# Optimization experiments

Measured on AMD Instinct MI355X. Metric: run time of the kernel, lower is better.

The kernel has to match this reference:

```python
import jax, jax.numpy as jnp
import numpy as np

B, C, S = 256, 1024, 14   # batch, channels, spatial (frozen by y.view(b,c,14,14))
C2 = 15                   # channels2 in the module
CAT = C // 2 * 3 + C2     # 1551 = 15 + 512 + 1024
EPS = 1e-5


def _conv(x, w, b, groups, pad):
    out = jax.lax.conv_general_dilated(
        x, w, window_strides=(1, 1), padding=((pad, pad), (pad, pad)),
        dimension_numbers=('NCHW', 'OIHW', 'NCHW'), feature_group_count=groups)
    return out + b[None, :, None, None]


def _bn(x, gamma, beta):
    # training-mode BatchNorm2d: biased batch stats over (N,H,W)
    m = x.mean((0, 2, 3), keepdims=True)
    v = x.var((0, 2, 3), keepdims=True)
    return (x - m) * jax.lax.rsqrt(v + EPS) * gamma[None, :, None, None] + beta[None, :, None, None]


def setup_inputs() -> dict:
    key = jax.random.key(0)
    ks = jax.random.split(key, 16)
    r = C2 // 7  # = 2
    inp = {
        'y': jax.random.normal(ks[0], (B, C2, S * S), jnp.float32),
        'x': jax.random.normal(ks[1], (B, C, S, S), jnp.float32),
        'fc1_w': jax.random.normal(ks[2], (r, C2), jnp.float32) * 0.2,
        'fc2_w': jax.random.normal(ks[3], (C2, r), jnp.float32) * 0.2,
        'conv_w': jax.random.normal(ks[4], (C // 2, C, 1, 1), jnp.float32) * 0.03,
        'conv_b': jnp.zeros((C // 2,), jnp.float32),
        'dconv_w': jax.random.normal(ks[5], (C, 1, 3, 3), jnp.float32) * 0.2,
        'dconv_b': jnp.zeros((C,), jnp.float32),
        'dw1_w': jax.random.normal(ks[6], (CAT, 1, 3, 3), jnp.float32) * 0.2,
        'dw1_b': jnp.zeros((CAT,), jnp.float32),
        'pw1_w': jax.random.normal(ks[7], (C // 2, CAT, 1, 1), jnp.float32) * 0.03,
        'pw1_b': jnp.zeros((C // 2,), jnp.float32),
        'gamma': jnp.ones((C // 2,), jnp.float32),
        'beta': jnp.zeros((C // 2,), jnp.float32),
        'n': 0,
    }
    return inp


def reference(y, x, fc1_w, fc2_w, conv_w, conv_b, dconv_w, dconv_b,
              dw1_w, dw1_b, pw1_w, pw1_b, gamma, beta, n):
    b = y.shape[0]
    y4 = y.reshape(b, C2, S, S)
    # SE block on the 15 sub-channels
    g = y4.mean((2, 3))                              # (b, 15) global avg pool
    h = jax.nn.relu(g @ fc1_w.T) @ fc2_w.T           # (b, 15)
    y1 = y4 * jax.nn.sigmoid(h)[:, :, None, None]
    # depthwise conv on x, then per-(b,c) row covariance of the 14x14 map
    x1 = _conv(x, dconv_w, dconv_b, C, 1)            # (b, C, 14, 14)
    x2 = jax.lax.stop_gradient(x1)                   # .detach() in the original
    xc = x2 - x2.mean(-1, keepdims=True)             # np.cov: rows=vars, cols=obs
    cov = jnp.einsum('bcik,bcjk->bcij', xc, xc) / (S - 1)
    z = _conv(cov, conv_w, conv_b, 1, 0)             # 1x1 conv C -> C//2
    z = jax.nn.sigmoid(_bn(z, gamma, beta))
    for _ in range(n):                               # n=0 at these shapes
        y1 = jax.image.resize(y1, (y1.shape[0], y1.shape[1], y1.shape[2] * 2, y1.shape[3] * 2), 'bilinear')
    cat = jnp.concatenate([y1, z, x], axis=1)        # (b, 1551, 14, 14)
    o = _conv(cat, dw1_w, dw1_b, CAT, 1)             # depthwise 3x3
    o = _conv(o, pw1_w, pw1_b, 1, 0)                 # pointwise 1x1 -> C//2
    return jax.nn.relu(_bn(o, gamma, beta))
```

## Files before the change

kernel.cpp:

```cpp
#include <hip/hip_runtime.h>

typedef unsigned int u32;
typedef unsigned short u16;
typedef __attribute__((ext_vector_type(8))) short bf16x8;
typedef __attribute__((ext_vector_type(4))) float f32x4;
typedef __attribute__((ext_vector_type(4))) u32 u32x4;

#define EPSBN 1e-5f

#define GLDS16(gp, lp) __builtin_amdgcn_global_load_lds( \
    (const __attribute__((address_space(1))) u32*)(gp), \
    (__attribute__((address_space(3))) u32*)(lp), 16, 0, 0)

#define OFF_ADW    0ull
#define OFF_COVT   0ull
#define OFF_S      160563200ull
#define OFF_WBZ    160578560ull
#define OFF_WBP    161627136ull
#define OFF_STATSZ 163265536ull
#define OFF_STATSO 163269632ull
#define OFF_SCZ    163273728ull
#define OFF_SHZ    163275776ull
#define OFF_SCO    163277824ull
#define OFF_SHO    163279872ull

static __device__ __forceinline__ float bf2f(u16 h){
  u32 u = ((u32)h) << 16; float f; __builtin_memcpy(&f, &u, 4); return f;
}
static __device__ __forceinline__ u16 f2bf(float f){
  u32 u; __builtin_memcpy(&u, &f, 4);
  u = (u + 0x7fffu + ((u >> 16) & 1u)) >> 16;
  return (u16)u;
}

__global__ __launch_bounds__(64) void se_kernel(const float* __restrict__ y,
    const float* __restrict__ fc1, const float* __restrict__ fc2, float* __restrict__ sse){
  __shared__ float g[15];
  __shared__ float t[2];
  int b = blockIdx.x, l = threadIdx.x;
  for (int c = 0; c < 15; ++c){
    float p = 0.f;
    for (int k = l; k < 196; k += 64) p += y[((size_t)b*15 + c)*196 + k];
    p += __shfl_xor(p, 32); p += __shfl_xor(p, 16); p += __shfl_xor(p, 8);
    p += __shfl_xor(p, 4);  p += __shfl_xor(p, 2);  p += __shfl_xor(p, 1);
    if (l == 0) g[c] = p * (1.f/196.f);
  }
  __syncthreads();
  if (l < 2){
    float a = 0.f;
    for (int c = 0; c < 15; ++c) a += g[c] * fc1[l*15 + c];
    t[l] = fmaxf(a, 0.f);
  }
  __syncthreads();
  if (l < 15){
    float h = t[0]*fc2[l*2] + t[1]*fc2[l*2+1];
    sse[b*15 + l] = 1.f / (1.f + __expf(-h));
  }
}

__global__ void wconv_kernel(const float* __restrict__ cw, const float* __restrict__ pw,
                             u16* __restrict__ wbz, u16* __restrict__ wbp){
  u32 stride = gridDim.x * blockDim.x;
  for (u32 i = blockIdx.x*blockDim.x + threadIdx.x; i < 524288u; i += stride)
    wbz[i] = f2bf(cw[i]);
  for (u32 i = blockIdx.x*blockDim.x + threadIdx.x; i < 819200u; i += stride){
    u32 n = i / 1600u, k = i - n*1600u;
    wbp[i] = f2bf(k < 1551u ? pw[(size_t)n*1551 + k] : 0.f);
  }
}

static __device__ __forceinline__ void dw3x3_row(const float* __restrict__ m,
    int i, const float* __restrict__ w, float bias, float* __restrict__ ov){
  float r[3][14];
  #pragma unroll
  for (int d = 0; d < 3; ++d){
    int rr = i + d - 1;
    if (rr >= 0 && rr < 14){
      #pragma unroll
      for (int k = 0; k < 14; ++k) r[d][k] = m[rr*14 + k];
    } else {
      #pragma unroll
      for (int k = 0; k < 14; ++k) r[d][k] = 0.f;
    }
  }
  #pragma unroll
  for (int k = 0; k < 14; ++k){
    float a = bias;
    #pragma unroll
    for (int dy = 0; dy < 3; ++dy){
      #pragma unroll
      for (int dx = 0; dx < 3; ++dx){
        int kk = k + dx - 1;
        if (kk >= 0 && kk < 14) a += w[dy*3+dx] * r[dy][kk];
      }
    }
    ov[k] = a;
  }
}

__global__ __launch_bounds__(256,5) void cov_kernel(const float* __restrict__ x,
    const float* __restrict__ dcw, const float* __restrict__ dcb, u16* __restrict__ covT){
  __shared__ __align__(16) float xs[16*200];
  __shared__ __align__(16) u32 xcb[16*132];
  __shared__ float wls[16][9];
  __shared__ float wlb[16];
  u32* covL32 = (u32*)xs;

  int tid = threadIdx.x;
  int c0 = blockIdx.x * 16, b = blockIdx.y;

  {
    const float4* xg = (const float4*)(x + ((size_t)b*1024 + c0)*196);
    for (int i = tid; i < 784; i += 256){
      float4 v = xg[i];
      u32 c = (u32)i / 49u, p4 = (u32)i - c*49u;
      *(float4*)&xs[c*200u + p4*4u] = v;
    }
  }
  if (tid < 144) wls[tid/9][tid%9] = dcw[(size_t)(c0 + tid/9)*9 + (tid%9)];
  if (tid < 16) wlb[tid] = dcb[c0 + tid];
  __syncthreads();

  {
    int c = tid >> 4, i = tid & 15;
    u32 q[8];
    #pragma unroll
    for (int j = 0; j < 8; ++j) q[j] = 0u;
    if (i < 14){
      float wr[9];
      #pragma unroll
      for (int qq = 0; qq < 9; ++qq) wr[qq] = wls[c][qq];
      float topm = (i > 0) ? 1.f : 0.f, botm = (i < 13) ? 1.f : 0.f;
      wr[0] *= topm; wr[1] *= topm; wr[2] *= topm;
      wr[6] *= botm; wr[7] *= botm; wr[8] *= botm;
      float bb = wlb[c];
      float rr[3][16];
      #pragma unroll
      for (int d = 0; d < 3; ++d){
        rr[d][0] = 0.f; rr[d][15] = 0.f;
        int rowr = i + d - 1;
        rowr = rowr < 0 ? 0 : (rowr > 13 ? 13 : rowr);
        const float* src = &xs[c*200 + rowr*14];
        #pragma unroll
        for (int j = 0; j < 7; ++j)
          *(float2*)&rr[d][1 + 2*j] = *(const float2*)&src[2*j];
      }
      float ov[14];
      #pragma unroll
      for (int k = 0; k < 14; ++k){
        float a = bb;
        #pragma unroll
        for (int dy = 0; dy < 3; ++dy)
          #pragma unroll
          for (int dx = 0; dx < 3; ++dx)
            a += wr[dy*3+dx] * rr[dy][k + dx];
        ov[k] = a;
      }
      float mean = 0.f;
      #pragma unroll
      for (int k = 0; k < 14; ++k) mean += ov[k];
      mean *= (1.f/14.f);
      #pragma unroll
      for (int j = 0; j < 7; ++j){
        u32 lo = f2bf(ov[2*j]   - mean);
        u32 hi = f2bf(ov[2*j+1] - mean);
        q[j] = lo | (hi << 16);
      }
    }
    u32x4 q0 = {q[0], q[1], q[2], q[3]};
    u32x4 q1 = {q[4], q[5], q[6], q[7]};
    *(u32x4*)&xcb[c*132 + i*8]     = q0;
    *(u32x4*)&xcb[c*132 + i*8 + 4] = q1;
  }
  __syncthreads();

  {
    int w = tid >> 6, l = tid & 63, lr = l & 15, lq = l >> 4;
    #pragma unroll
    for (int pp = 0; pp < 2; ++pp){
      int clo = w*4 + 2*pp;
      bf16x8 alo = {0,0,0,0,0,0,0,0}, ahi = {0,0,0,0,0,0,0,0};
      if (lq < 2){
        alo = *(const bf16x8*)&xcb[clo*132 + lr*8 + lq*4];
        ahi = *(const bf16x8*)&xcb[(clo+1)*132 + lr*8 + lq*4];
      }
      f32x4 dlo = {0.f,0.f,0.f,0.f}, dhi = {0.f,0.f,0.f,0.f};
      dlo = __builtin_amdgcn_mfma_f32_16x16x32_bf16(alo, alo, dlo, 0, 0, 0);
      dhi = __builtin_amdgcn_mfma_f32_16x16x32_bf16(ahi, ahi, dhi, 0, 0, 0);
      if (lr < 14){
        int cp = w*2 + pp;
        #pragma unroll
        for (int r = 0; r < 4; ++r){
          int rowi = lq*4 + r;
          if (rowi < 14){
            u32 vv = (u32)f2bf(dlo[r] * (1.f/13.f)) | ((u32)f2bf(dhi[r] * (1.f/13.f)) << 16);
            covL32[cp*210 + rowi*14 + lr] = vv;
          }
        }
      }
    }
  }
  __syncthreads();

  for (int i = tid; i < 1568; i += 256){
    int cp = i & 7, ij = i >> 3;
    u32 v = covL32[cp*210 + ij];
    *(u32*)(covT + ((size_t)(b*196 + ij)*1024 + c0 + 2*cp)) = v;
  }
}

__global__ __launch_bounds__(256,5) void adw_kernel(
    const float* __restrict__ y, const float* __restrict__ sse,
    const u16* __restrict__ zraw, const float* __restrict__ scz, const float* __restrict__ shz,
    const float* __restrict__ x, const float* __restrict__ dw1w, const float* __restrict__ dw1b,
    u16* __restrict__ Adw){
  __shared__ __align__(16) float ms[32*201 + 4];
  __shared__ float wd[32][9];
  __shared__ float bd[32];
  int tid = threadIdx.x;
  int cc0 = blockIdx.x * 32, b = blockIdx.y;

  for (int i = tid; i < 288; i += 256){
    int c = i / 9, q = i - c*9;
    int cc = cc0 + c;
    wd[c][q] = (cc < 1551) ? dw1w[(size_t)cc*9 + q] : 0.f;
  }
  if (tid < 32) bd[tid] = (cc0 + tid < 1551) ? dw1b[cc0 + tid] : 0.f;

  if (cc0 < 15){
    int ny = 15 - cc0; if (ny > 32) ny = 32;
    for (int i = tid; i < ny*196; i += 256){
      u32 c = (u32)i / 196u, p = (u32)i - c*196u;
      int cc = cc0 + (int)c;
      ms[c*201u + p] = y[((size_t)b*15 + cc)*196 + p] * sse[b*15 + cc];
    }
  }
  {
    int zs = cc0 > 15 ? cc0 : 15;
    int ze = cc0 + 32 < 527 ? cc0 + 32 : 527;
    if (zs < ze){
      int nz = ze - zs, lbase = zs - cc0, obase = zs - 15;
      for (int i = tid; i < nz*196; i += 256){
        int oo = i % nz, p = i / nz;
        int o = obase + oo;
        float v = bf2f(zraw[((size_t)b*196 + p)*512 + o]);
        v = v * scz[o] + shz[o];
        v = 1.f / (1.f + __expf(-v));
        ms[(u32)(lbase + oo)*201u + p] = v;
      }
    }
  }
  {
    int xs_ = cc0 > 527 ? cc0 : 527;
    int xe = cc0 + 32 < 1551 ? cc0 + 32 : 1551;
    if (xs_ < xe){
      int nx = xe - xs_, lbase = xs_ - cc0, cxs = xs_ - 527;
      for (int i = tid; i < nx*196; i += 256){
        u32 c = (u32)i / 196u, p = (u32)i - c*196u;
        ms[(u32)(lbase + (int)c)*201u + p] = x[((size_t)b*1024 + cxs + c)*196 + p];
      }
    }
  }
  {
    int ps = cc0 > 1551 ? cc0 : 1551;
    int pe = cc0 + 32;
    if (ps < pe){
      int np = pe - ps, lbase = ps - cc0;
      for (int i = tid; i < np*196; i += 256){
        u32 c = (u32)i / 196u, p = (u32)i - c*196u;
        ms[(u32)(lbase + (int)c)*201u + p] = 0.f;
      }
    }
  }
  __syncthreads();

  for (int t = tid; t < 448; t += 256){
    int cc = t & 31, i = t >> 5;
    float ov[14];
    dw3x3_row(&ms[cc*201], i, &wd[cc][0], bd[cc], ov);
    size_t obase = ((size_t)b*196 + i*14) * 1600 + cc0 + cc;
    #pragma unroll
    for (int k = 0; k < 14; ++k) Adw[obase + (size_t)k*1600] = f2bf(ov[k]);
  }
}

template<int MODE>
__global__ __launch_bounds__(256,3) void gemm_kernel(
    const u16* __restrict__ A, const u16* __restrict__ Bw,
    const float* __restrict__ bias, void* __restrict__ outp,
    float* __restrict__ stats, int K){
  __shared__ __align__(16) char smem[33280];
  u16* As = (u16*)smem;
  u16* Bs = (u16*)(smem + 16384);

  int tid = threadIdx.x;
  int w = tid >> 6, l = tid & 63;
  int wm = w >> 1, wn = w & 1;
  int lr = l & 15, lq = l >> 4;
  int m0 = blockIdx.y * 128;
  int n0 = blockIdx.x * 128;

  f32x4 acc[4][4] = {};
  int kTiles = K >> 6;

  for (int kt = 0; kt < kTiles; ++kt){
    if (kt) __syncthreads();
    #pragma unroll
    for (int i = 0; i < 4; ++i){
      int s = tid + i*256;
      int row = s >> 3, c8 = s & 7, sc = c8 ^ (row & 7);
      GLDS16(A  + (size_t)(m0 + row)*K + kt*64 + sc*8, As + s*8);
      GLDS16(Bw + (size_t)(n0 + row)*K + kt*64 + sc*8, Bs + s*8);
    }
    __syncthreads();
    #pragma unroll
    for (int ks = 0; ks < 2; ++ks){
      bf16x8 af[4], bfv[4];
      #pragma unroll
      for (int mi = 0; mi < 4; ++mi){
        int row = wm*64 + mi*16 + lr;
        int q = (ks*4 + lq) ^ (row & 7);
        af[mi] = *(const bf16x8*)(As + row*64 + q*8);
      }
      #pragma unroll
      for (int ni = 0; ni < 4; ++ni){
        int row = wn*64 + ni*16 + lr;
        int q = (ks*4 + lq) ^ (row & 7);
        bfv[ni] = *(const bf16x8*)(Bs + row*64 + q*8);
      }
      #pragma unroll
      for (int mi = 0; mi < 4; ++mi)
        #pragma unroll
        for (int ni = 0; ni < 4; ++ni)
          acc[mi][ni] = __builtin_amdgcn_mfma_f32_16x16x32_bf16(af[mi], bfv[ni], acc[mi][ni], 0, 0, 0);
    }
  }

  #pragma unroll
  for (int ni = 0; ni < 4; ++ni){
    int col = n0 + wn*64 + ni*16 + lr;
    float bb = bias[col];
    float s1 = 0.f, s2 = 0.f;
    #pragma unroll
    for (int mi = 0; mi < 4; ++mi)
      #pragma unroll
      for (int r = 0; r < 4; ++r){
        float v = acc[mi][ni][r] + bb;
        acc[mi][ni][r] = v;
        s1 += v; s2 += v*v;
      }
    s1 += __shfl_xor(s1, 16); s1 += __shfl_xor(s1, 32);
    s2 += __shfl_xor(s2, 16); s2 += __shfl_xor(s2, 32);
    if (lq == 0){
      atomicAdd(&stats[col], s1);
      atomicAdd(&stats[512 + col], s2);
    }
  }

  if (MODE == 0){
    u16* zo = (u16*)outp;
    #pragma unroll
    for (int mi = 0; mi < 4; ++mi)
      #pragma unroll
      for (int r = 0; r < 4; ++r){
        int m = m0 + wm*64 + mi*16 + lq*4 + r;
        size_t base = (size_t)m*512 + n0 + wn*64 + lr;
        #pragma unroll
        for (int ni = 0; ni < 4; ++ni)
          zo[base + ni*16] = f2bf(acc[mi][ni][r]);
      }
  } else {
    __syncthreads();
    float* eb = (float*)smem;
    #pragma unroll
    for (int rnd = 0; rnd < 2; ++rnd){
      if (wm == rnd){
        float* e = eb + wn * (64*65);
        #pragma unroll
        for (int mi = 0; mi < 4; ++mi)
          #pragma unroll
          for (int ni = 0; ni < 4; ++ni)
            #pragma unroll
            for (int r = 0; r < 4; ++r)
              e[(mi*16 + lq*4 + r)*65 + ni*16 + lr] = acc[mi][ni][r];
        int m = m0 + wm*64 + l;
        u32 bq = (u32)m / 196u;
        u32 ij = (u32)m - bq*196u;
        float* ob = (float*)outp + ((size_t)bq*512 + n0 + wn*64)*196 + ij;
        #pragma unroll 8
        for (int no = 0; no < 64; ++no)
          ob[(size_t)no*196] = e[l*65 + no];
      }
      __syncthreads();
    }
  }
}

__global__ void bnprep_kernel(const float* __restrict__ stats, const float* __restrict__ gamma,
    const float* __restrict__ beta, float* __restrict__ sc, float* __restrict__ sh){
  int o = threadIdx.x;
  float m = stats[o] * (1.f/50176.f);
  float v = stats[512+o] * (1.f/50176.f) - m*m;
  float inv = rsqrtf(v + EPSBN);
  float g = gamma[o] * inv;
  sc[o] = g;
  sh[o] = beta[o] - m*g;
}

__global__ void final_kernel(float4* __restrict__ o4, const float* __restrict__ sc,
                             const float* __restrict__ sh){
  u32 stride = gridDim.x * blockDim.x;
  for (u32 i = blockIdx.x*blockDim.x + threadIdx.x; i < 6422528u; i += stride){
    u32 oc = (i / 49u) & 511u;
    float s = sc[oc], t = sh[oc];
    float4 v = o4[i];
    v.x = fmaxf(fmaf(v.x, s, t), 0.f);
    v.y = fmaxf(fmaf(v.y, s, t), 0.f);
    v.z = fmaxf(fmaf(v.z, s, t), 0.f);
    v.w = fmaxf(fmaf(v.w, s, t), 0.f);
    o4[i] = v;
  }
}

extern "C" void kernel_launch(void* const* d_in, const int* in_sizes, int n_in,
                              void* d_out, int out_size, void* d_ws, size_t ws_size,
                              hipStream_t stream){
  (void)in_sizes; (void)n_in; (void)out_size; (void)ws_size;
  const float* y      = (const float*)d_in[0];
  const float* x      = (const float*)d_in[1];
  const float* fc1    = (const float*)d_in[2];
  const float* fc2    = (const float*)d_in[3];
  const float* convw  = (const float*)d_in[4];
  const float* convb  = (const float*)d_in[5];
  const float* dconvw = (const float*)d_in[6];
  const float* dconvb = (const float*)d_in[7];
  const float* dw1w   = (const float*)d_in[8];
  const float* dw1b   = (const float*)d_in[9];
  const float* pw1w   = (const float*)d_in[10];
  const float* pw1b   = (const float*)d_in[11];
  const float* gamma  = (const float*)d_in[12];
  const float* beta   = (const float*)d_in[13];

  char* ws = (char*)d_ws;
  u16* covT   = (u16*)(ws + OFF_COVT);
  u16* Adw    = (u16*)(ws + OFF_ADW);
  float* sse  = (float*)(ws + OFF_S);
  u16* wbz    = (u16*)(ws + OFF_WBZ);
  u16* wbp    = (u16*)(ws + OFF_WBP);
  float* statsZ = (float*)(ws + OFF_STATSZ);
  float* statsO = (float*)(ws + OFF_STATSO);
  float* scz  = (float*)(ws + OFF_SCZ);
  float* shz  = (float*)(ws + OFF_SHZ);
  float* sco  = (float*)(ws + OFF_SCO);
  float* sho  = (float*)(ws + OFF_SHO);
  u16* zraw   = (u16*)d_out;
  float* outf = (float*)d_out;

  hipMemsetAsync(statsZ, 0, 8192, stream);
  se_kernel<<<256, 64, 0, stream>>>(y, fc1, fc2, sse);
  wconv_kernel<<<2048, 256, 0, stream>>>(convw, pw1w, wbz, wbp);
  cov_kernel<<<dim3(64, 256), 256, 0, stream>>>(x, dconvw, dconvb, covT);
  gemm_kernel<0><<<dim3(4, 392), 256, 0, stream>>>(covT, wbz, convb, (void*)zraw, statsZ, 1024);
  bnprep_kernel<<<1, 512, 0, stream>>>(statsZ, gamma, beta, scz, shz);
  adw_kernel<<<dim3(50, 256), 256, 0, stream>>>(y, sse, zraw, scz, shz, x, dw1w, dw1b, Adw);
  gemm_kernel<1><<<dim3(4, 392), 256, 0, stream>>>(Adw, wbp, pw1b, (void*)outf, statsO, 1600);
  bnprep_kernel<<<1, 512, 0, stream>>>(statsO, gamma, beta, sco, sho);
  final_kernel<<<8192, 256, 0, stream>>>((float4*)outf, sco, sho);
}
```

Before: 542.1 us.

## Store z channel-major and vectorize adw staging and depthwise stencil

The first GEMM now writes its bf16 z output transposed (channel-major, stride 50176) through the LDS epilogue, the same path the second GEMM already uses. This lets adw_kernel read z as contiguous pixel pairs per channel instead of strided gathers across 512-wide rows. adw also loads x with float4 and pads the LDS row stride to 202 so float2 accesses stay aligned. The 3x3 depthwise stencil uses zero-padded register rows with masked weights instead of per-element branches. The cost is that the z GEMM epilogue now goes through LDS, and its global stores are strided per lane (coalesced across lanes only along m).

```diff
diff --git a/kernel.cpp b/kernel.cpp
--- a/kernel.cpp
+++ b/kernel.cpp
@@ -69,35 +69,6 @@
   }
 }
 
-static __device__ __forceinline__ void dw3x3_row(const float* __restrict__ m,
-    int i, const float* __restrict__ w, float bias, float* __restrict__ ov){
-  float r[3][14];
-  #pragma unroll
-  for (int d = 0; d < 3; ++d){
-    int rr = i + d - 1;
-    if (rr >= 0 && rr < 14){
-      #pragma unroll
-      for (int k = 0; k < 14; ++k) r[d][k] = m[rr*14 + k];
-    } else {
-      #pragma unroll
-      for (int k = 0; k < 14; ++k) r[d][k] = 0.f;
-    }
-  }
-  #pragma unroll
-  for (int k = 0; k < 14; ++k){
-    float a = bias;
-    #pragma unroll
-    for (int dy = 0; dy < 3; ++dy){
-      #pragma unroll
-      for (int dx = 0; dx < 3; ++dx){
-        int kk = k + dx - 1;
-        if (kk >= 0 && kk < 14) a += w[dy*3+dx] * r[dy][kk];
-      }
-    }
-    ov[k] = a;
-  }
-}
-
 __global__ __launch_bounds__(256,5) void cov_kernel(const float* __restrict__ x,
     const float* __restrict__ dcw, const float* __restrict__ dcb, u16* __restrict__ covT){
   __shared__ __align__(16) float xs[16*200];
@@ -211,10 +182,10 @@
 
 __global__ __launch_bounds__(256,5) void adw_kernel(
     const float* __restrict__ y, const float* __restrict__ sse,
-    const u16* __restrict__ zraw, const float* __restrict__ scz, const float* __restrict__ shz,
+    const u16* __restrict__ zT, const float* __restrict__ scz, const float* __restrict__ shz,
     const float* __restrict__ x, const float* __restrict__ dw1w, const float* __restrict__ dw1b,
     u16* __restrict__ Adw){
-  __shared__ __align__(16) float ms[32*201 + 4];
+  __shared__ __align__(16) float ms[32*202];
   __shared__ float wd[32][9];
   __shared__ float bd[32];
   int tid = threadIdx.x;
@@ -228,11 +199,10 @@
   if (tid < 32) bd[tid] = (cc0 + tid < 1551) ? dw1b[cc0 + tid] : 0.f;
 
   if (cc0 < 15){
-    int ny = 15 - cc0; if (ny > 32) ny = 32;
+    int ny = 15;
     for (int i = tid; i < ny*196; i += 256){
       u32 c = (u32)i / 196u, p = (u32)i - c*196u;
-      int cc = cc0 + (int)c;
-      ms[c*201u + p] = y[((size_t)b*15 + cc)*196 + p] * sse[b*15 + cc];
+      ms[c*202u + p] = y[((size_t)b*15 + c)*196 + p] * sse[b*15 + c];
     }
   }
   {
@@ -240,13 +210,18 @@
     int ze = cc0 + 32 < 527 ? cc0 + 32 : 527;
     if (zs < ze){
       int nz = ze - zs, lbase = zs - cc0, obase = zs - 15;
-      for (int i = tid; i < nz*196; i += 256){
-        int oo = i % nz, p = i / nz;
-        int o = obase + oo;
-        float v = bf2f(zraw[((size_t)b*196 + p)*512 + o]);
-        v = v * scz[o] + shz[o];
-        v = 1.f / (1.f + __expf(-v));
-        ms[(u32)(lbase + oo)*201u + p] = v;
+      const u16* zrow = zT + (size_t)obase*50176 + (size_t)b*196;
+      for (int i = tid; i < nz*98; i += 256){
+        u32 oo = (u32)i / 98u, pp = (u32)i - oo*98u;
+        u32 v = *(const u32*)(zrow + (size_t)oo*50176 + pp*2u);
+        int o = obase + (int)oo;
+        float s = scz[o], h = shz[o];
+        float v0 = bf2f((u16)(v & 0xffffu)) * s + h;
+        float v1 = bf2f((u16)(v >> 16))     * s + h;
+        v0 = 1.f / (1.f + __expf(-v0));
+        v1 = 1.f / (1.f + __expf(-v1));
+        float2 fv = {v0, v1};
+        *(float2*)&ms[(u32)(lbase + (int)oo)*202u + pp*2u] = fv;
       }
     }
   }
@@ -255,9 +230,14 @@
     int xe = cc0 + 32 < 1551 ? cc0 + 32 : 1551;
     if (xs_ < xe){
       int nx = xe - xs_, lbase = xs_ - cc0, cxs = xs_ - 527;
-      for (int i = tid; i < nx*196; i += 256){
-        u32 c = (u32)i / 196u, p = (u32)i - c*196u;
-        ms[(u32)(lbase + (int)c)*201u + p] = x[((size_t)b*1024 + cxs + c)*196 + p];
+      const float4* xg = (const float4*)(x + ((size_t)b*1024 + cxs)*196);
+      for (int i = tid; i < nx*49; i += 256){
+        float4 v = xg[i];
+        u32 c = (u32)i / 49u, p4 = (u32)i - c*49u;
+        float* dst = &ms[(u32)(lbase + (int)c)*202u + p4*4u];
+        float2 lo = {v.x, v.y}, hi = {v.z, v.w};
+        *(float2*)dst = lo;
+        *(float2*)(dst + 2) = hi;
       }
     }
   }
@@ -268,7 +248,7 @@
       int np = pe - ps, lbase = ps - cc0;
       for (int i = tid; i < np*196; i += 256){
         u32 c = (u32)i / 196u, p = (u32)i - c*196u;
-        ms[(u32)(lbase + (int)c)*201u + p] = 0.f;
+        ms[(u32)(lbase + (int)c)*202u + p] = 0.f;
       }
     }
   }
@@ -276,11 +256,35 @@
 
   for (int t = tid; t < 448; t += 256){
     int cc = t & 31, i = t >> 5;
-    float ov[14];
-    dw3x3_row(&ms[cc*201], i, &wd[cc][0], bd[cc], ov);
+    float wr[9];
+    #pragma unroll
+    for (int qq = 0; qq < 9; ++qq) wr[qq] = wd[cc][qq];
+    float topm = (i > 0) ? 1.f : 0.f, botm = (i < 13) ? 1.f : 0.f;
+    wr[0] *= topm; wr[1] *= topm; wr[2] *= topm;
+    wr[6] *= botm; wr[7] *= botm; wr[8] *= botm;
+    float bb = bd[cc];
+    float rr[3][16];
+    #pragma unroll
+    for (int d = 0; d < 3; ++d){
+      rr[d][0] = 0.f; rr[d][15] = 0.f;
+      int rowr = i + d - 1;
+      rowr = rowr < 0 ? 0 : (rowr > 13 ? 13 : rowr);
+      const float* src = &ms[cc*202 + rowr*14];
+      #pragma unroll
+      for (int j = 0; j < 7; ++j)
+        *(float2*)&rr[d][1 + 2*j] = *(const float2*)&src[2*j];
+    }
     size_t obase = ((size_t)b*196 + i*14) * 1600 + cc0 + cc;
     #pragma unroll
-    for (int k = 0; k < 14; ++k) Adw[obase + (size_t)k*1600] = f2bf(ov[k]);
+    for (int k = 0; k < 14; ++k){
+      float a = bb;
+      #pragma unroll
+      for (int dy = 0; dy < 3; ++dy)
+        #pragma unroll
+        for (int dx = 0; dx < 3; ++dx)
+          a += wr[dy*3+dx] * rr[dy][k + dx];
+      Adw[obase + (size_t)k*1600] = f2bf(a);
+    }
   }
 }
 
@@ -357,33 +361,26 @@
     }
   }
 
-  if (MODE == 0){
-    u16* zo = (u16*)outp;
-    #pragma unroll
-    for (int mi = 0; mi < 4; ++mi)
-      #pragma unroll
-      for (int r = 0; r < 4; ++r){
-        int m = m0 + wm*64 + mi*16 + lq*4 + r;
-        size_t base = (size_t)m*512 + n0 + wn*64 + lr;
+  __syncthreads();
+  float* eb = (float*)smem;
+  #pragma unroll
+  for (int rnd = 0; rnd < 2; ++rnd){
+    if (wm == rnd){
+      float* e = eb + wn * (64*65);
+      #pragma unroll
+      for (int mi = 0; mi < 4; ++mi)
         #pragma unroll
         for (int ni = 0; ni < 4; ++ni)
-          zo[base + ni*16] = f2bf(acc[mi][ni][r]);
-      }
-  } else {
-    __syncthreads();
-    float* eb = (float*)smem;
-    #pragma unroll
-    for (int rnd = 0; rnd < 2; ++rnd){
-      if (wm == rnd){
-        float* e = eb + wn * (64*65);
-        #pragma unroll
-        for (int mi = 0; mi < 4; ++mi)
           #pragma unroll
-          for (int ni = 0; ni < 4; ++ni)
-            #pragma unroll
-            for (int r = 0; r < 4; ++r)
-              e[(mi*16 + lq*4 + r)*65 + ni*16 + lr] = acc[mi][ni][r];
-        int m = m0 + wm*64 + l;
+          for (int r = 0; r < 4; ++r)
+            e[(mi*16 + lq*4 + r)*65 + ni*16 + lr] = acc[mi][ni][r];
+      int m = m0 + wm*64 + l;
+      if (MODE == 0){
+        u16* ob = (u16*)outp + (size_t)(n0 + wn*64)*50176 + m;
+        #pragma unroll 8
+        for (int no = 0; no < 64; ++no)
+          ob[(size_t)no*50176] = f2bf(e[l*65 + no]);
+      } else {
         u32 bq = (u32)m / 196u;
         u32 ij = (u32)m - bq*196u;
         float* ob = (float*)outp + ((size_t)bq*512 + n0 + wn*64)*196 + ij;
@@ -391,8 +388,8 @@
         for (int no = 0; no < 64; ++no)
           ob[(size_t)no*196] = e[l*65 + no];
       }
-      __syncthreads();
-    }
+    }
+    __syncthreads();
   }
 }
 
@@ -453,16 +450,16 @@
   float* shz  = (float*)(ws + OFF_SHZ);
   float* sco  = (float*)(ws + OFF_SCO);
   float* sho  = (float*)(ws + OFF_SHO);
-  u16* zraw   = (u16*)d_out;
+  u16* zT     = (u16*)d_out;
   float* outf = (float*)d_out;
 
   hipMemsetAsync(statsZ, 0, 8192, stream);
   se_kernel<<<256, 64, 0, stream>>>(y, fc1, fc2, sse);
   wconv_kernel<<<2048, 256, 0, stream>>>(convw, pw1w, wbz, wbp);
   cov_kernel<<<dim3(64, 256), 256, 0, stream>>>(x, dconvw, dconvb, covT);
-  gemm_kernel<0><<<dim3(4, 392), 256, 0, stream>>>(covT, wbz, convb, (void*)zraw, statsZ, 1024);
+  gemm_kernel<0><<<dim3(4, 392), 256, 0, stream>>>(covT, wbz, convb, (void*)zT, statsZ, 1024);
   bnprep_kernel<<<1, 512, 0, stream>>>(statsZ, gamma, beta, scz, shz);
-  adw_kernel<<<dim3(50, 256), 256, 0, stream>>>(y, sse, zraw, scz, shz, x, dw1w, dw1b, Adw);
+  adw_kernel<<<dim3(50, 256), 256, 0, stream>>>(y, sse, zT, scz, shz, x, dw1w, dw1b, Adw);
   gemm_kernel<1><<<dim3(4, 392), 256, 0, stream>>>(Adw, wbp, pw1b, (void*)outf, statsO, 1600);
   bnprep_kernel<<<1, 512, 0, stream>>>(statsO, gamma, beta, sco, sho);
   final_kernel<<<8192, 256, 0, stream>>>((float4*)outf, sco, sho);
```

Measured after the change: 524.3 us. -3.3%, faster.
